# Kernel optimization log

Hardware: AMD Instinct MI355X
Metric: run time of the kernel (lower is better)

The kernel has to match this reference:

```python
import jax, jax.numpy as jnp
import numpy as np

B, C, H, W = 2, 128, 48, 48
NUM_HEADS = 8


def dct_matrix(N):
    # Orthonormal DCT-II matrix: D[k, n] = s_k * cos(pi * (n + 0.5) * k / N)
    n = np.arange(N)
    D = np.cos(np.pi * (n[None, :] + 0.5) * n[:, None] / N) * np.sqrt(2.0 / N)
    D[0] *= 1.0 / np.sqrt(2.0)
    return jnp.asarray(D, dtype=jnp.float32)


def setup_inputs() -> dict:
    key = jax.random.key(0)
    ks = jax.random.split(key, 10)
    w_scale = 1.0 / np.sqrt(C)  # kaiming-ish init for 1x1 convs
    inp = {
        "freq_feat": jax.random.normal(ks[0], (B, C, H, W), dtype=jnp.float32),
        "spatial_feat": jax.random.normal(ks[1], (B, C, H, W), dtype=jnp.float32),
        "Wq": jax.random.normal(ks[2], (C, C), dtype=jnp.float32) * w_scale,
        "bq": jnp.zeros((C,), dtype=jnp.float32),
        "Wk": jax.random.normal(ks[3], (C, C), dtype=jnp.float32) * w_scale,
        "bk": jnp.zeros((C,), dtype=jnp.float32),
        "Wv": jax.random.normal(ks[4], (C, C), dtype=jnp.float32) * w_scale,
        "bv": jnp.zeros((C,), dtype=jnp.float32),
        "Wo": jax.random.normal(ks[5], (C, C), dtype=jnp.float32) * w_scale,
        "bo": jnp.zeros((C,), dtype=jnp.float32),
    }
    return inp


def _proj(x, Wm, b):
    # 1x1 conv == channel-mixing GEMM
    return jnp.einsum('oc,bchw->bohw', Wm, x) + b[None, :, None, None]


def reference(freq_feat, spatial_feat, Wq, bq, Wk, bk, Wv, bv, Wo, bo):
    b, c, h, w = freq_feat.shape
    nh = NUM_HEADS
    d = c // nh
    L = h * w

    # 2D orthonormal DCT-II of the spatial features
    DH = dct_matrix(h)
    DW = dct_matrix(w)
    spatial_freq = jnp.einsum('hm,bcmn,wn->bchw', DH, spatial_feat, DW)

    Q = _proj(freq_feat, Wq, bq)
    K = _proj(spatial_freq, Wk, bk)
    V = _proj(spatial_freq, Wv, bv)

    # (B, C, H, W) -> (B, nh, L, d)
    def to_heads(x):
        return x.reshape(b, nh, d, L).transpose(0, 1, 3, 2)

    Qh, Kh, Vh = to_heads(Q), to_heads(K), to_heads(V)

    scale = 1.0 / np.sqrt(d)
    scores = jnp.einsum('bhld,bhsd->bhls', Qh, Kh) * scale  # (B, nh, L, L)
    attn = jax.nn.softmax(scores, axis=-1)
    out = jnp.einsum('bhls,bhsd->bhld', attn, Vh)  # (B, nh, L, d)

    out = out.transpose(0, 1, 3, 2).reshape(b, c, h, w)
    return _proj(out, Wo, bo)
```

## Files before the change

### kernel.cpp

```cpp
#include <hip/hip_runtime.h>
#include <math.h>

#define L_TOT 2304
#define C_TOT 128

typedef float v4f  __attribute__((ext_vector_type(4)));
typedef __bf16 v8bf __attribute__((ext_vector_type(8)));
typedef __bf16 v4bf __attribute__((ext_vector_type(4)));

#define MFMA_16x16x32_BF16(A, B, C) __builtin_amdgcn_mfma_f32_16x16x32_bf16((A), (B), (C), 0, 0, 0)

__device__ __forceinline__ void async_cp16(const __bf16* g, __bf16* l){
  __builtin_amdgcn_global_load_lds((const __attribute__((address_space(1))) unsigned int*)g,
                                   (__attribute__((address_space(3))) unsigned int*)l,
                                   16, 0, 0);
}

template<int MODE>
__device__ __forceinline__ void mfma_proj(const float* __restrict__ W,
                                          const float* __restrict__ bias,
                                          const float* __restrict__ Xb,
                                          float* __restrict__ Yf,
                                          __bf16* __restrict__ Yh,
                                          int n0, __bf16* Bhi, int tid){
  __bf16* Blo = Bhi + 4352;
  const int wave = tid >> 6, lane = tid & 63, qd = lane >> 4, cn = lane & 15;
  const int m0 = wave * 32;
  v8bf ahi[2][4], alo[2][4];
  #pragma unroll
  for (int rt = 0; rt < 2; rt++)
    #pragma unroll
    for (int ks = 0; ks < 4; ks++){
      const float* wp = W + (size_t)(m0 + rt * 16 + cn) * C_TOT + ks * 32 + qd * 8;
      float4 w0 = *(const float4*)wp;
      float4 w1 = *(const float4*)(wp + 4);
      float wv[8] = {w0.x, w0.y, w0.z, w0.w, w1.x, w1.y, w1.z, w1.w};
      #pragma unroll
      for (int j = 0; j < 8; j++){
        __bf16 h = (__bf16)wv[j];
        ahi[rt][ks][j] = h;
        alo[rt][ks][j] = (__bf16)(wv[j] - (float)h);
      }
    }
  {
    int k = tid >> 1, nh = tid & 1;
    const float* xp = Xb + (size_t)k * L_TOT + n0 + nh * 16;
    float4 x0 = *(const float4*)xp;
    float4 x1 = *(const float4*)(xp + 4);
    float4 x2 = *(const float4*)(xp + 8);
    float4 x3 = *(const float4*)(xp + 12);
    float xv[16] = {x0.x, x0.y, x0.z, x0.w, x1.x, x1.y, x1.z, x1.w,
                    x2.x, x2.y, x2.z, x2.w, x3.x, x3.y, x3.z, x3.w};
    #pragma unroll
    for (int i = 0; i < 16; i++){
      __bf16 h = (__bf16)xv[i];
      int row = nh * 16 + i;
      Bhi[row * 136 + k] = h;
      Blo[row * 136 + k] = (__bf16)(xv[i] - (float)h);
    }
  }
  __syncthreads();
  v4f acc[2][2];
  #pragma unroll
  for (int rt = 0; rt < 2; rt++)
    #pragma unroll
    for (int ct = 0; ct < 2; ct++) acc[rt][ct] = (v4f){0.f, 0.f, 0.f, 0.f};
  #pragma unroll
  for (int ks = 0; ks < 4; ks++){
    v8bf bhi[2], blo[2];
    #pragma unroll
    for (int ct = 0; ct < 2; ct++){
      bhi[ct] = *(const v8bf*)&Bhi[(ct * 16 + cn) * 136 + ks * 32 + qd * 8];
      blo[ct] = *(const v8bf*)&Blo[(ct * 16 + cn) * 136 + ks * 32 + qd * 8];
    }
    #pragma unroll
    for (int rt = 0; rt < 2; rt++)
      #pragma unroll
      for (int ct = 0; ct < 2; ct++){
        acc[rt][ct] = MFMA_16x16x32_BF16(ahi[rt][ks], bhi[ct], acc[rt][ct]);
        acc[rt][ct] = MFMA_16x16x32_BF16(ahi[rt][ks], blo[ct], acc[rt][ct]);
        acc[rt][ct] = MFMA_16x16x32_BF16(alo[rt][ks], bhi[ct], acc[rt][ct]);
      }
  }
  #pragma unroll
  for (int rt = 0; rt < 2; rt++){
    float bv[4];
    #pragma unroll
    for (int r = 0; r < 4; r++) bv[r] = bias[m0 + rt * 16 + qd * 4 + r];
    #pragma unroll
    for (int ct = 0; ct < 2; ct++){
      int col = n0 + ct * 16 + cn;
      if (MODE == 0){
        #pragma unroll
        for (int r = 0; r < 4; r++)
          Yf[(size_t)(m0 + rt * 16 + qd * 4 + r) * L_TOT + col] = acc[rt][ct][r] + bv[r];
      } else if (MODE == 1){
        v4bf kk;
        #pragma unroll
        for (int r = 0; r < 4; r++) kk[r] = (__bf16)((acc[rt][ct][r] + bv[r]) * 0.25f);
        *(v4bf*)&Yh[(size_t)col * C_TOT + m0 + rt * 16 + qd * 4] = kk;
      } else {
        #pragma unroll
        for (int r = 0; r < 4; r++)
          Yh[(size_t)(m0 + rt * 16 + qd * 4 + r) * L_TOT + col] = (__bf16)(acc[rt][ct][r] + bv[r]);
      }
    }
  }
}

__global__ __launch_bounds__(256) void k_front(const float* __restrict__ spat,
                                               float* __restrict__ SF,
                                               const float* __restrict__ freq,
                                               const float* __restrict__ Wq,
                                               const float* __restrict__ bq,
                                               float* __restrict__ Qo){
  __shared__ __align__(16) unsigned char smraw[37632];
  int blk = blockIdx.x, tid = threadIdx.x;
  if (blk < 256){
    float* Ds  = (float*)smraw;
    float* DTs = Ds + 2352;
    float* Xs  = Ds + 4704;
    float* Ts  = Ds + 7056;
    const float* Xi = spat + (size_t)blk * 2304;
    float* Fi = SF + (size_t)blk * 2304;
    for (int i = tid; i < 2304; i += 256){
      int k = i / 48, n = i - k * 48;
      int m = ((2 * n + 1) * k) % 192;
      float v = cosf(0.032724923474893679f * (float)m) * 0.204124145231931508f;
      if (k == 0) v *= 0.707106781186547524f;
      Ds[k * 49 + n] = v;
      DTs[n * 49 + k] = v;
      Xs[k * 49 + n] = Xi[i];
    }
    __syncthreads();
    int tr = (tid >> 4) * 3, tc = (tid & 15) * 3;
    {
      float a[3][3] = {};
      for (int n = 0; n < 48; n++){
        float x0 = Xs[tr * 49 + n], x1 = Xs[(tr + 1) * 49 + n], x2 = Xs[(tr + 2) * 49 + n];
        float d0 = DTs[n * 49 + tc], d1 = DTs[n * 49 + tc + 1], d2 = DTs[n * 49 + tc + 2];
        a[0][0] += x0 * d0; a[0][1] += x0 * d1; a[0][2] += x0 * d2;
        a[1][0] += x1 * d0; a[1][1] += x1 * d1; a[1][2] += x1 * d2;
        a[2][0] += x2 * d0; a[2][1] += x2 * d1; a[2][2] += x2 * d2;
      }
      #pragma unroll
      for (int i = 0; i < 3; i++)
        #pragma unroll
        for (int j = 0; j < 3; j++)
          Ts[(tr + i) * 49 + tc + j] = a[i][j];
    }
    __syncthreads();
    {
      float c[3][3] = {};
      for (int m = 0; m < 48; m++){
        float d0 = Ds[tr * 49 + m], d1 = Ds[(tr + 1) * 49 + m], d2 = Ds[(tr + 2) * 49 + m];
        float t0 = Ts[m * 49 + tc], t1 = Ts[m * 49 + tc + 1], t2 = Ts[m * 49 + tc + 2];
        c[0][0] += d0 * t0; c[0][1] += d0 * t1; c[0][2] += d0 * t2;
        c[1][0] += d1 * t0; c[1][1] += d1 * t1; c[1][2] += d1 * t2;
        c[2][0] += d2 * t0; c[2][1] += d2 * t1; c[2][2] += d2 * t2;
      }
      #pragma unroll
      for (int i = 0; i < 3; i++)
        #pragma unroll
        for (int j = 0; j < 3; j++)
          Fi[(tr + i) * 48 + tc + j] = c[i][j];
    }
  } else {
    int idx = blk - 256;
    int b = idx / 72, n0 = (idx % 72) * 32;
    mfma_proj<0>(Wq, bq, freq + (size_t)b * C_TOT * L_TOT,
                 Qo + (size_t)b * C_TOT * L_TOT, (__bf16*)0, n0, (__bf16*)smraw, tid);
  }
}

__global__ __launch_bounds__(256) void k_kv(const float* __restrict__ SF,
                                            const float* __restrict__ Wk, const float* __restrict__ bk,
                                            const float* __restrict__ Wv, const float* __restrict__ bv,
                                            __bf16* __restrict__ KT, __bf16* __restrict__ Vg){
  __shared__ __align__(16) unsigned char smraw[17408];
  int b = blockIdx.z, n0 = blockIdx.x * 32;
  const float* Xb = SF + (size_t)b * C_TOT * L_TOT;
  if (blockIdx.y == 0)
    mfma_proj<1>(Wk, bk, Xb, (float*)0, KT + (size_t)b * L_TOT * C_TOT, n0, (__bf16*)smraw, threadIdx.x);
  else
    mfma_proj<2>(Wv, bv, Xb, (float*)0, Vg + (size_t)b * C_TOT * L_TOT, n0, (__bf16*)smraw, threadIdx.x);
}

__global__ __launch_bounds__(256) void k_oproj(const float* __restrict__ AO,
                                               const float* __restrict__ Wo, const float* __restrict__ bo,
                                               float* __restrict__ out){
  __shared__ __align__(16) unsigned char smraw[17408];
  int b = blockIdx.y, n0 = blockIdx.x * 32;
  mfma_proj<0>(Wo, bo, AO + (size_t)b * C_TOT * L_TOT,
               out + (size_t)b * C_TOT * L_TOT, (__bf16*)0, n0, (__bf16*)smraw, threadIdx.x);
}

__global__ __launch_bounds__(256) void k_attn(const float* __restrict__ Q,
                                              const __bf16* __restrict__ KT,
                                              const __bf16* __restrict__ V,
                                              float* __restrict__ AO){
  const int L = L_TOT;
  int bh = blockIdx.y;
  int b = bh >> 3, h = bh & 7;
  int c0 = h * 16;
  const float*  Qb  = Q  + ((size_t)b * C_TOT + c0) * L;
  const __bf16* KTb = KT + (size_t)b * L * C_TOT;
  const __bf16* Vb  = V  + ((size_t)b * C_TOT + c0) * L;
  int tid = threadIdx.x;
  int wave = tid >> 6, lane = tid & 63;
  int qd = lane >> 4, cn = lane & 15;
  int l0 = blockIdx.x * 64;

  __shared__ __align__(16) __bf16 smem[8192 + 8192 + 2560];
  __bf16* Kt  = smem;
  __bf16* Vs  = smem + 8192;
  __bf16* Ptw = smem + 16384 + wave * 640;

  v8bf qf[4];
  #pragma unroll
  for (int t = 0; t < 4; t++){
    #pragma unroll
    for (int j = 0; j < 8; j++) qf[t][j] = (__bf16)0.0f;
  }
  if (qd < 2){
    #pragma unroll
    for (int t = 0; t < 4; t++)
      #pragma unroll
      for (int j = 0; j < 8; j++)
        qf[t][j] = (__bf16)Qb[(size_t)(qd * 8 + j) * L + l0 + t * 16 + cn];
  }

  v4f acc[4];
  float den[4] = {0.f, 0.f, 0.f, 0.f};
  #pragma unroll
  for (int t = 0; t < 4; t++) acc[t] = (v4f){0.f, 0.f, 0.f, 0.f};

  for (int ch = 0; ch < 5; ch++){
    int s0 = ch * 512;
    int cnt = (ch == 4) ? 256 : 512;
    __syncthreads();
    {
      int per = (cnt >> 5) >> 2;
      for (int jj = 0; jj < per; jj++){
        int j = wave * per + jj;
        int s = j * 32 + (lane >> 1);
        async_cp16(KTb + (size_t)(s0 + s) * C_TOT + c0 + (lane & 1) * 8,
                   Kt + j * 512);
      }
      if (cnt == 512){
        #pragma unroll
        for (int jj = 0; jj < 4; jj++){
          int d = wave * 4 + jj;
          async_cp16(Vb + (size_t)d * L + s0 + ((lane ^ (d & 7)) << 3),
                     Vs + d * 512);
        }
      } else {
        int d = tid >> 4, og = tid & 15;
        const __bf16* gp = Vb + (size_t)d * L + s0 + og * 16;
        v8bf v0 = *(const v8bf*)gp;
        v8bf v1 = *(const v8bf*)(gp + 8);
        int pd = d & 7;
        *(v8bf*)&Vs[d * 512 + (((og * 2)     ^ pd) << 3)] = v0;
        *(v8bf*)&Vs[d * 512 + (((og * 2 + 1) ^ pd) << 3)] = v1;
      }
    }
    __syncthreads();

    int nsu = cnt >> 7;
    int wbase = wave * (cnt >> 2);
    for (int su = 0; su < nsu; su++){
      int sb = wbase + su * 32;
      v8bf a0, a1;
      #pragma unroll
      for (int j = 0; j < 8; j++){ a0[j] = (__bf16)0.0f; a1[j] = (__bf16)0.0f; }
      if (qd < 2){
        a0 = *(const v8bf*)&Kt[(sb + cn) * 16 + qd * 8];
        a1 = *(const v8bf*)&Kt[(sb + 16 + cn) * 16 + qd * 8];
      }
      int jv = sb >> 3;
      v8bf vf = *(const v8bf*)&Vs[cn * 512 + (((jv + qd) ^ (cn & 7)) << 3)];
      #pragma unroll
      for (int t = 0; t < 4; t++){
        v4f z = {0.f, 0.f, 0.f, 0.f};
        v4f st0 = MFMA_16x16x32_BF16(a0, qf[t], z);
        v4f st1 = MFMA_16x16x32_BF16(a1, qf[t], z);
        float p0[4], p1[4];
        #pragma unroll
        for (int i = 0; i < 4; i++){
          p0[i] = __expf(st0[i]); den[t] += p0[i];
          p1[i] = __expf(st1[i]); den[t] += p1[i];
        }
        v4bf w0, w1;
        #pragma unroll
        for (int i = 0; i < 4; i++){ w0[i] = (__bf16)p0[i]; w1[i] = (__bf16)p1[i]; }
        *(v4bf*)&Ptw[cn * 40 + qd * 4]      = w0;
        *(v4bf*)&Ptw[cn * 40 + 16 + qd * 4] = w1;
        v8bf pf = *(const v8bf*)&Ptw[cn * 40 + qd * 8];
        acc[t] = MFMA_16x16x32_BF16(vf, pf, acc[t]);
      }
    }
  }

  __syncthreads();
  float* redA = (float*)smem;
  float* redD = (float*)(smem + 8192);
  #pragma unroll
  for (int t = 0; t < 4; t++){
    *(v4f*)&redA[((wave * 4 + t) * 64 + lane) * 4] = acc[t];
    redD[(wave * 4 + t) * 64 + lane] = den[t];
  }
  __syncthreads();
  {
    int t = wave;
    v4f a = (v4f){0.f, 0.f, 0.f, 0.f};
    float dn = 0.f;
    #pragma unroll
    for (int w2 = 0; w2 < 4; w2++){
      v4f xx = *(const v4f*)&redA[((w2 * 4 + t) * 64 + lane) * 4];
      a[0] += xx[0]; a[1] += xx[1]; a[2] += xx[2]; a[3] += xx[3];
      dn += redD[(w2 * 4 + t) * 64 + lane];
    }
    dn += __shfl_xor(dn, 16);
    dn += __shfl_xor(dn, 32);
    float inv = 1.0f / dn;
    float* Ao = AO + ((size_t)b * C_TOT + c0) * L;
    #pragma unroll
    for (int r2 = 0; r2 < 4; r2++)
      Ao[(size_t)(qd * 4 + r2) * L + l0 + t * 16 + cn] = a[r2] * inv;
  }
}

extern "C" void kernel_launch(void* const* d_in, const int* in_sizes, int n_in,
                              void* d_out, int out_size, void* d_ws, size_t ws_size,
                              hipStream_t stream){
  const float* freq = (const float*)d_in[0];
  const float* spat = (const float*)d_in[1];
  const float* Wq = (const float*)d_in[2]; const float* bq = (const float*)d_in[3];
  const float* Wk = (const float*)d_in[4]; const float* bk = (const float*)d_in[5];
  const float* Wv = (const float*)d_in[6]; const float* bv = (const float*)d_in[7];
  const float* Wo = (const float*)d_in[8]; const float* bo = (const float*)d_in[9];
  float* ws = (float*)d_ws;

  float* SF = ws;
  float* Qb = ws + 589824;
  float* AO = ws + 1179648;
  __bf16* KTg = (__bf16*)(ws + 1769472);
  __bf16* Vg  = (__bf16*)(ws + 2064384);
  float* out = (float*)d_out;

  k_front<<<dim3(400), dim3(256), 0, stream>>>(spat, SF, freq, Wq, bq, Qb);
  k_kv<<<dim3(72, 2, 2), dim3(256), 0, stream>>>(SF, Wk, bk, Wv, bv, KTg, Vg);
  k_attn<<<dim3(36, 16), dim3(256), 0, stream>>>(Qb, KTg, Vg, AO);
  k_oproj<<<dim3(72, 2), dim3(256), 0, stream>>>(AO, Wo, bo, out);
}
```

Before: 126.1 us.

## Store Q transposed and attention output in bf16 to cut intermediate traffic

The Q projection now writes bf16 in an L-major (transposed) layout, so the attention kernel can load each Q fragment as one 16-byte vector instead of eight strided fp32 loads. The attention output is also stored as bf16, and the output projection gets a dedicated kernel that reads this bf16 activation, transposes it through LDS and runs only hi/lo weight-split MFMAs. This halves the size of the Q and attention-output intermediates and simplifies the loads. In exchange, the attention output is rounded to bf16 before the final projection, which loses some precision.

```diff
diff --git a/kernel.cpp b/kernel.cpp
--- a/kernel.cpp
+++ b/kernel.cpp
@@ -22,6 +22,7 @@
                                           const float* __restrict__ Xb,
                                           float* __restrict__ Yf,
                                           __bf16* __restrict__ Yh,
+                                          float scale,
                                           int n0, __bf16* Bhi, int tid){
   __bf16* Blo = Bhi + 4352;
   const int wave = tid >> 6, lane = tid & 63, qd = lane >> 4, cn = lane & 15;
@@ -97,7 +98,7 @@
       } else if (MODE == 1){
         v4bf kk;
         #pragma unroll
-        for (int r = 0; r < 4; r++) kk[r] = (__bf16)((acc[rt][ct][r] + bv[r]) * 0.25f);
+        for (int r = 0; r < 4; r++) kk[r] = (__bf16)((acc[rt][ct][r] + bv[r]) * scale);
         *(v4bf*)&Yh[(size_t)col * C_TOT + m0 + rt * 16 + qd * 4] = kk;
       } else {
         #pragma unroll
@@ -113,7 +114,7 @@
                                                const float* __restrict__ freq,
                                                const float* __restrict__ Wq,
                                                const float* __restrict__ bq,
-                                               float* __restrict__ Qo){
+                                               __bf16* __restrict__ QT){
   __shared__ __align__(16) unsigned char smraw[37632];
   int blk = blockIdx.x, tid = threadIdx.x;
   if (blk < 256){
@@ -168,8 +169,8 @@
   } else {
     int idx = blk - 256;
     int b = idx / 72, n0 = (idx % 72) * 32;
-    mfma_proj<0>(Wq, bq, freq + (size_t)b * C_TOT * L_TOT,
-                 Qo + (size_t)b * C_TOT * L_TOT, (__bf16*)0, n0, (__bf16*)smraw, tid);
+    mfma_proj<1>(Wq, bq, freq + (size_t)b * C_TOT * L_TOT,
+                 (float*)0, QT + (size_t)b * L_TOT * C_TOT, 1.0f, n0, (__bf16*)smraw, tid);
   }
 }
 
@@ -181,29 +182,91 @@
   int b = blockIdx.z, n0 = blockIdx.x * 32;
   const float* Xb = SF + (size_t)b * C_TOT * L_TOT;
   if (blockIdx.y == 0)
-    mfma_proj<1>(Wk, bk, Xb, (float*)0, KT + (size_t)b * L_TOT * C_TOT, n0, (__bf16*)smraw, threadIdx.x);
+    mfma_proj<1>(Wk, bk, Xb, (float*)0, KT + (size_t)b * L_TOT * C_TOT, 0.25f, n0, (__bf16*)smraw, threadIdx.x);
   else
-    mfma_proj<2>(Wv, bv, Xb, (float*)0, Vg + (size_t)b * C_TOT * L_TOT, n0, (__bf16*)smraw, threadIdx.x);
-}
-
-__global__ __launch_bounds__(256) void k_oproj(const float* __restrict__ AO,
+    mfma_proj<2>(Wv, bv, Xb, (float*)0, Vg + (size_t)b * C_TOT * L_TOT, 1.0f, n0, (__bf16*)smraw, threadIdx.x);
+}
+
+__global__ __launch_bounds__(256) void k_oproj(const __bf16* __restrict__ AO,
                                                const float* __restrict__ Wo, const float* __restrict__ bo,
                                                float* __restrict__ out){
-  __shared__ __align__(16) unsigned char smraw[17408];
+  __shared__ __align__(16) __bf16 Bs[32 * 136];
   int b = blockIdx.y, n0 = blockIdx.x * 32;
-  mfma_proj<0>(Wo, bo, AO + (size_t)b * C_TOT * L_TOT,
-               out + (size_t)b * C_TOT * L_TOT, (__bf16*)0, n0, (__bf16*)smraw, threadIdx.x);
-}
-
-__global__ __launch_bounds__(256) void k_attn(const float* __restrict__ Q,
+  int tid = threadIdx.x;
+  const int wave = tid >> 6, lane = tid & 63, qd = lane >> 4, cn = lane & 15;
+  const int m0 = wave * 32;
+  v8bf ahi[2][4], alo[2][4];
+  #pragma unroll
+  for (int rt = 0; rt < 2; rt++)
+    #pragma unroll
+    for (int ks = 0; ks < 4; ks++){
+      const float* wp = Wo + (size_t)(m0 + rt * 16 + cn) * C_TOT + ks * 32 + qd * 8;
+      float4 w0 = *(const float4*)wp;
+      float4 w1 = *(const float4*)(wp + 4);
+      float wv[8] = {w0.x, w0.y, w0.z, w0.w, w1.x, w1.y, w1.z, w1.w};
+      #pragma unroll
+      for (int j = 0; j < 8; j++){
+        __bf16 h = (__bf16)wv[j];
+        ahi[rt][ks][j] = h;
+        alo[rt][ks][j] = (__bf16)(wv[j] - (float)h);
+      }
+    }
+  {
+    int k = tid >> 1, nh = tid & 1;
+    const __bf16* src = AO + ((size_t)b * C_TOT + k) * L_TOT + n0 + nh * 16;
+    v8bf x0 = *(const v8bf*)src;
+    v8bf x1 = *(const v8bf*)(src + 8);
+    #pragma unroll
+    for (int i = 0; i < 8; i++){
+      Bs[(nh * 16 + i) * 136 + k] = x0[i];
+      Bs[(nh * 16 + 8 + i) * 136 + k] = x1[i];
+    }
+  }
+  __syncthreads();
+  v4f acc[2][2];
+  #pragma unroll
+  for (int rt = 0; rt < 2; rt++)
+    #pragma unroll
+    for (int ct = 0; ct < 2; ct++) acc[rt][ct] = (v4f){0.f, 0.f, 0.f, 0.f};
+  #pragma unroll
+  for (int ks = 0; ks < 4; ks++){
+    v8bf bf[2];
+    #pragma unroll
+    for (int ct = 0; ct < 2; ct++)
+      bf[ct] = *(const v8bf*)&Bs[(ct * 16 + cn) * 136 + ks * 32 + qd * 8];
+    #pragma unroll
+    for (int rt = 0; rt < 2; rt++)
+      #pragma unroll
+      for (int ct = 0; ct < 2; ct++){
+        acc[rt][ct] = MFMA_16x16x32_BF16(ahi[rt][ks], bf[ct], acc[rt][ct]);
+        acc[rt][ct] = MFMA_16x16x32_BF16(alo[rt][ks], bf[ct], acc[rt][ct]);
+      }
+  }
+  float* ob = out + (size_t)b * C_TOT * L_TOT;
+  #pragma unroll
+  for (int rt = 0; rt < 2; rt++){
+    float bv[4];
+    #pragma unroll
+    for (int r = 0; r < 4; r++) bv[r] = bo[m0 + rt * 16 + qd * 4 + r];
+    #pragma unroll
+    for (int ct = 0; ct < 2; ct++){
+      int col = n0 + ct * 16 + cn;
+      #pragma unroll
+      for (int r = 0; r < 4; r++)
+        ob[(size_t)(m0 + rt * 16 + qd * 4 + r) * L_TOT + col] = acc[rt][ct][r] + bv[r];
+    }
+  }
+}
+
+__global__ __launch_bounds__(256) void k_attn(const __bf16* __restrict__ QT,
                                               const __bf16* __restrict__ KT,
                                               const __bf16* __restrict__ V,
-                                              float* __restrict__ AO){
+                                              __bf16* __restrict__ AO){
   const int L = L_TOT;
   int bh = blockIdx.y;
   int b = bh >> 3, h = bh & 7;
   int c0 = h * 16;
-  const float*  Qb  = Q  + ((size_t)b * C_TOT + c0) * L;
+  const __bf16* QTb = QT + (size_t)b * L * C_TOT;
   const __bf16* KTb = KT + (size_t)b * L * C_TOT;
   const __bf16* Vb  = V  + ((size_t)b * C_TOT + c0) * L;
   int tid = threadIdx.x;
@@ -225,9 +288,7 @@
   if (qd < 2){
     #pragma unroll
     for (int t = 0; t < 4; t++)
-      #pragma unroll
-      for (int j = 0; j < 8; j++)
-        qf[t][j] = (__bf16)Qb[(size_t)(qd * 8 + j) * L + l0 + t * 16 + cn];
+      qf[t] = *(const v8bf*)&QTb[(size_t)(l0 + t * 16 + cn) * C_TOT + c0 + qd * 8];
   }
 
   v4f acc[4];
@@ -323,10 +384,10 @@
     dn += __shfl_xor(dn, 16);
     dn += __shfl_xor(dn, 32);
     float inv = 1.0f / dn;
-    float* Ao = AO + ((size_t)b * C_TOT + c0) * L;
+    __bf16* Ao = AO + ((size_t)b * C_TOT + c0) * L;
     #pragma unroll
     for (int r2 = 0; r2 < 4; r2++)
-      Ao[(size_t)(qd * 4 + r2) * L + l0 + t * 16 + cn] = a[r2] * inv;
+      Ao[(size_t)(qd * 4 + r2) * L + l0 + t * 16 + cn] = (__bf16)(a[r2] * inv);
   }
 }
 
@@ -341,15 +402,15 @@
   const float* Wo = (const float*)d_in[8]; const float* bo = (const float*)d_in[9];
   float* ws = (float*)d_ws;
 
-  float* SF = ws;
-  float* Qb = ws + 589824;
-  float* AO = ws + 1179648;
-  __bf16* KTg = (__bf16*)(ws + 1769472);
-  __bf16* Vg  = (__bf16*)(ws + 2064384);
+  float* SF   = ws;
+  __bf16* QTg = (__bf16*)(ws + 589824);
+  __bf16* AOg = (__bf16*)(ws + 884736);
+  __bf16* KTg = (__bf16*)(ws + 1179648);
+  __bf16* Vg  = (__bf16*)(ws + 1474560);
   float* out = (float*)d_out;
 
-  k_front<<<dim3(400), dim3(256), 0, stream>>>(spat, SF, freq, Wq, bq, Qb);
+  k_front<<<dim3(400), dim3(256), 0, stream>>>(spat, SF, freq, Wq, bq, QTg);
   k_kv<<<dim3(72, 2, 2), dim3(256), 0, stream>>>(SF, Wk, bk, Wv, bv, KTg, Vg);
-  k_attn<<<dim3(36, 16), dim3(256), 0, stream>>>(Qb, KTg, Vg, AO);
-  k_oproj<<<dim3(72, 2), dim3(256), 0, stream>>>(AO, Wo, bo, out);
-}
+  k_attn<<<dim3(36, 16), dim3(256), 0, stream>>>(QTg, KTg, Vg, AOg);
+  k_oproj<<<dim3(72, 2), dim3(256), 0, stream>>>(AOg, Wo, bo, out);
+}
```

Measured after the change: 124.6 us. No clear change (-1.2%).
